# Kernel tuning notes

Hardware: AMD Instinct MI355X
Metric: run time of the kernel (lower is better)

Reference implementation:

```python
import jax, jax.numpy as jnp
import numpy as np

DM = 1024        # model dim
E = 32           # totalexperts = expertsets*nexperts = 8*4
FE = 128         # expertsize
T = 4            # sparsity = nexperts (tokens per group)
EPS_TIEBREAK = 1e-6


def setup_inputs() -> dict:
    key = jax.random.key(0)
    k0, k1, k2, k3 = jax.random.split(key, 4)
    x = jax.random.normal(k0, (4, 4096, DM), dtype=jnp.float32)
    # fan_in-style inits matching misc.get_init_weight / get_init_bias
    controller = jax.random.normal(k1, (DM, E), dtype=jnp.float32) / np.float32(np.sqrt(DM))
    f1 = jax.random.normal(k2, (DM, E, FE), dtype=jnp.float32) / np.float32(np.sqrt(DM))
    bias = jnp.zeros((E, FE), dtype=jnp.float32)
    f2 = jax.random.normal(k3, (E, FE, DM), dtype=jnp.float32) / np.float32(np.sqrt(E * FE / T))
    return {"x": x, "controller": controller, "f1": f1, "bias": bias, "f2": f2}


def reference(x, controller, f1, bias, f2):
    B, S, d = x.shape
    t = T
    g = S // t
    # '... (b t) d -> ... b t d'
    grouped = x.reshape(B, g, t, d)
    # controller logits: '... t d, d e -> ... t e'
    logits = jnp.einsum('bgtd,de->bgte', grouped, controller)
    # deterministic tie-break offset over the t (slot) axis
    logits = logits + jnp.linspace(0.0, EPS_TIEBREAK, t, dtype=logits.dtype)[:, None]
    # softmax over dim=1 (group axis) as in original
    probs = jax.nn.softmax(logits, axis=1)
    # hard argmax mask over dim=-3 (group axis), scaled by soft probs
    perm = (logits == jnp.max(logits, axis=1, keepdims=True)).astype(x.dtype) * probs
    # expert up-projection with soft permutation: '... t d, d e f, ... t e -> ... e f'
    inner = jnp.einsum('bgtd,def,bgte->bgef', grouped, f1, perm)
    inner = jax.nn.relu(inner + bias)
    # expert down-projection: '... e f, e f d -> ... e d'
    inter = jnp.einsum('bgef,efd->bged', inner, f2)
    # unpermute: '... e d, ... t e -> ... t d'
    res = jnp.einsum('bged,bgte->bgtd', inter, perm)
    return res.reshape(B, S, d)
```

## Files before the change

kernel.cpp:

```cpp
#include <hip/hip_runtime.h>
#include <math.h>


#define DM   1024
#define NE   32
#define FE   128
#define T4   4
#define SS   4096
#define NGRP 1024
#define NROW 512
#define LP_STRIDE (NROW * NGRP)
#define VP_OFF   524288
#define HH_OFF   1572864

__global__ __launch_bounds__(256, 4)
void k_logits(const float* __restrict__ x, const float* __restrict__ ctrl,
              float* __restrict__ Lp, float* __restrict__ out)
{
    const int m      = blockIdx.x;
    const int ks     = blockIdx.y;
    const int tid    = threadIdx.x;
    const int base_s = m * 64;
    const int b      = base_s >> 12;
    const int g0     = (base_s & 4095) >> 2;

    __shared__ float xT[64 * 68];
    __shared__ float cs[64 * 32];

    const int tq = tid & 15;
    const int eg = tid >> 4;

    float acc[4][2];
#pragma unroll
    for (int i = 0; i < 4; ++i) { acc[i][0] = 0.f; acc[i][1] = 0.f; }

    const int row0 = tid >> 2;
    const int f4i  = tid & 3;

    for (int kit = 0; kit < 4; ++kit) {
        const int k0 = ks * 256 + kit * 64;
        __syncthreads();
        {
            const float* xp = x + (size_t)(base_s + row0) * DM + k0;
#pragma unroll
            for (int cr = 0; cr < 4; ++cr) {
                const int col = f4i + cr * 4;
                const float4 v = *(const float4*)(xp + col * 4);
                const int d = col * 4;
                xT[(d + 0) * 68 + row0] = v.x;
                xT[(d + 1) * 68 + row0] = v.y;
                xT[(d + 2) * 68 + row0] = v.z;
                xT[(d + 3) * 68 + row0] = v.w;
            }
        }
        {
            const float4* cg = (const float4*)(ctrl + (size_t)k0 * NE);
            float4* cl = (float4*)cs;
            cl[tid]       = cg[tid];
            cl[tid + 256] = cg[tid + 256];
        }
        __syncthreads();
#pragma unroll 8
        for (int d = 0; d < 64; ++d) {
            const float4 xv = *(const float4*)(xT + d * 68 + tq * 4);
            const float2 cv = *(const float2*)(cs + d * 32 + eg * 2);
            const float xa[4] = { xv.x, xv.y, xv.z, xv.w };
#pragma unroll
            for (int i = 0; i < 4; ++i) {
                acc[i][0] += xa[i] * cv.x;
                acc[i][1] += xa[i] * cv.y;
            }
        }
    }

    {
        float* Lb = Lp + (size_t)ks * LP_STRIDE;
        const int g = g0 + tq;
#pragma unroll
        for (int i = 0; i < 4; ++i)
#pragma unroll
            for (int j = 0; j < 2; ++j) {
                const int row = (b * T4 + i) * NE + eg * 2 + j;
                Lb[(size_t)row * NGRP + g] = acc[i][j];
            }
    }

    {
        const float4 z = make_float4(0.f, 0.f, 0.f, 0.f);
        float4* o4 = (float4*)(out + (size_t)(base_s + ks * 16) * DM);
#pragma unroll 4
        for (int i = tid; i < 16 * DM / 4; i += 256) o4[i] = z;
    }
}

__global__ __launch_bounds__(128)
void k_route(float* __restrict__ Lp)
{
    const int r    = blockIdx.x * 2 + (threadIdx.x >> 6);
    const int lane = threadIdx.x & 63;
    const float* L0 = Lp + (size_t)r * NGRP;

    float mx = -INFINITY, s = 0.f;
    int gm = 0;
#pragma unroll
    for (int c = 0; c < 4; ++c) {
        const int g0c = c * 256 + lane * 4;
        const float4 v0 = *(const float4*)(L0 + g0c);
        const float4 v1 = *(const float4*)(L0 + 1 * LP_STRIDE + g0c);
        const float4 v2 = *(const float4*)(L0 + 2 * LP_STRIDE + g0c);
        const float4 v3 = *(const float4*)(L0 + 3 * LP_STRIDE + g0c);
        const float l[4] = { v0.x + v1.x + v2.x + v3.x,
                             v0.y + v1.y + v2.y + v3.y,
                             v0.z + v1.z + v2.z + v3.z,
                             v0.w + v1.w + v2.w + v3.w };
#pragma unroll
        for (int j = 0; j < 4; ++j) {
            const float lv = l[j];
            if (lv > mx) { s = s * __expf(mx - lv) + 1.f; mx = lv; gm = g0c + j; }
            else         { s += __expf(lv - mx); }
        }
    }
#pragma unroll
    for (int off = 1; off < 64; off <<= 1) {
        const float m2 = __shfl_xor(mx, off);
        const float s2 = __shfl_xor(s, off);
        const int   g2 = __shfl_xor(gm, off);
        const float mn = fmaxf(mx, m2);
        s  = s * __expf(mx - mn) + s2 * __expf(m2 - mn);
        gm = (m2 > mx) ? g2 : ((m2 == mx && g2 < gm) ? g2 : gm);
        mx = mn;
    }
    if (lane == 0) {
        ((int*)Lp)[(size_t)r * NGRP] = gm;
        Lp[(size_t)r * NGRP + 1] = 1.f / s;
    }
}

__global__ __launch_bounds__(256, 4)
void k_up(const float* __restrict__ x, const float* __restrict__ f1,
          float* __restrict__ ws)
{
    const int e   = blockIdx.x & 31;
    const int dc  = (blockIdx.x >> 5) & 15;
    const int rh  = blockIdx.x >> 9;
    const int tid = threadIdx.x;

    __shared__ float xs[8 * 68];
    __shared__ int   gS[8];

    if (tid < 8) {
        const int r = (rh * 8 + tid) * NE + e;
        gS[tid] = ((const int*)ws)[(size_t)r * NGRP];
    }
    __syncthreads();

    if (tid < 128) {
        const int row = tid >> 4;
        const int f4c = tid & 15;
        const int grow = rh * 8 + row;
        const int bq = grow >> 2, t = grow & 3;
        const int s = bq * SS + gS[row] * 4 + t;
        const float4 v = *(const float4*)(x + (size_t)s * DM + dc * 64 + f4c * 4);
        xs[row * 68 + f4c * 4 + 0] = v.x;
        xs[row * 68 + f4c * 4 + 1] = v.y;
        xs[row * 68 + f4c * 4 + 2] = v.z;
        xs[row * 68 + f4c * 4 + 3] = v.w;
    }
    __syncthreads();

    const int f4 = tid & 31;
    const int rw = tid >> 5;
    const float* f1p = f1 + (size_t)(dc * 64) * (NE * FE) + e * FE + f4 * 4;
    const float* xp  = xs + rw * 68;

    float a[4] = {0.f, 0.f, 0.f, 0.f};
#pragma unroll 16
    for (int dl = 0; dl < 64; ++dl) {
        const float4 w4 = *(const float4*)(f1p + (size_t)dl * (NE * FE));
        const float xa = xp[dl];
        a[0] += xa * w4.x; a[1] += xa * w4.y; a[2] += xa * w4.z; a[3] += xa * w4.w;
    }

    float* Vp = ws + VP_OFF + (size_t)(dc * 32 + e) * (16 * FE);
    *(float4*)(Vp + (rh * 8 + rw) * FE + f4 * 4) = make_float4(a[0], a[1], a[2], a[3]);
}

__global__ __launch_bounds__(256, 4)
void k_act(const float* __restrict__ bias, float* __restrict__ ws)
{
    const int e   = blockIdx.x & 31;
    const int b   = blockIdx.x >> 5;
    const int tid = threadIdx.x;

    __shared__ float vv[T4][FE];
    __shared__ int   gS[T4];
    __shared__ float pS[T4];

    if (tid < 4) {
        const int r = (b * T4 + tid) * NE + e;
        gS[tid] = ((const int*)ws)[(size_t)r * NGRP];
        pS[tid] = ws[(size_t)r * NGRP + 1];
    }

    const float* Vp = ws + VP_OFF;
#pragma unroll
    for (int q = 0; q < 2; ++q) {
        const int idx = tid + q * 256;
        const int t = idx >> 7, f = idx & 127;
        float s = 0.f;
#pragma unroll
        for (int dc = 0; dc < 16; ++dc)
            s += Vp[(size_t)(dc * 32 + e) * (16 * FE) + (b * T4 + t) * FE + f];
        vv[t][f] = s;
    }
    __syncthreads();

#pragma unroll
    for (int q = 0; q < 2; ++q) {
        const int idx = tid + q * 256;
        const int t = idx >> 7, f = idx & 127;
        float u = bias[e * FE + f];
#pragma unroll
        for (int t2 = 0; t2 < T4; ++t2)
            if (gS[t2] == gS[t]) u += pS[t2] * vv[t2][f];
        ws[HH_OFF + (size_t)e * (16 * FE) + (b * T4 + t) * FE + f] =
            pS[t] * fmaxf(u, 0.f);
    }
}

__global__ __launch_bounds__(256, 2)
void k_down(const float* __restrict__ f2, const float* __restrict__ ws,
            float* __restrict__ out)
{
    const int e   = blockIdx.x & 31;
    const int dt  = (blockIdx.x >> 5) & 7;
    const int rh  = blockIdx.x >> 8;
    const int tid = threadIdx.x;

    __shared__ float hs[8 * FE];
    __shared__ int   gS[8];

    if (tid < 8) {
        const int r = (rh * 8 + tid) * NE + e;
        gS[tid] = ((const int*)ws)[(size_t)r * NGRP];
    }
    {
        const int row = tid >> 5, f4 = tid & 31;
        const float4 v = *(const float4*)(ws + HH_OFF + (size_t)e * (16 * FE)
                                             + (rh * 8 + row) * FE + f4 * 4);
        *(float4*)(hs + row * FE + f4 * 4) = v;
    }
    __syncthreads();

    const int d4 = tid & 31;
    const int rw = tid >> 5;
    const float* f2p = f2 + (size_t)e * FE * DM + dt * 128 + d4 * 4;
    const float* hp  = hs + rw * FE;

    float a[4] = {0.f, 0.f, 0.f, 0.f};
#pragma unroll 16
    for (int f = 0; f < FE; ++f) {
        const float4 w4 = *(const float4*)(f2p + (size_t)f * DM);
        const float ha = hp[f];
        a[0] += ha * w4.x; a[1] += ha * w4.y; a[2] += ha * w4.z; a[3] += ha * w4.w;
    }

    const int grow = rh * 8 + rw;
    const int bq = grow >> 2, t = grow & 3;
    float* orow = out + ((size_t)(bq * SS + gS[rw] * 4 + t)) * DM + dt * 128 + d4 * 4;
    atomicAdd(orow + 0, a[0]);
    atomicAdd(orow + 1, a[1]);
    atomicAdd(orow + 2, a[2]);
    atomicAdd(orow + 3, a[3]);
}

extern "C" void kernel_launch(void* const* d_in, const int* in_sizes, int n_in,
                              void* d_out, int out_size, void* d_ws, size_t ws_size,
                              hipStream_t stream)
{
    const float* x    = (const float*)d_in[0];
    const float* ctrl = (const float*)d_in[1];
    const float* f1   = (const float*)d_in[2];
    const float* bias = (const float*)d_in[3];
    const float* f2   = (const float*)d_in[4];
    float* out = (float*)d_out;
    float* ws  = (float*)d_ws;

    k_logits<<<dim3(256, 4), 256, 0, stream>>>(x, ctrl, ws, out);
    k_route <<<dim3(256),    128, 0, stream>>>(ws);
    k_up    <<<dim3(1024),   256, 0, stream>>>(x, f1, ws);
    k_act   <<<dim3(128),    256, 0, stream>>>(bias, ws);
    k_down  <<<dim3(512),    256, 0, stream>>>(f2, ws, out);
}
```

Baseline: 193.1 us.

## Fuse activation into down-projection, retile logits with prefetch, split route blocks

Removes the separate k_act kernel by having each k_down block reduce the partial up-projection sums, apply the soft-permutation mix, bias and ReLU into shared memory before the down-projection. k_logits now computes 128 rows by 4 experts per thread group and register-prefetches the next x/controller tile, so global loads overlap the previous tile's compute. k_route runs one row per 64-thread block. The fusion repeats the activation reduction across the 8 dt blocks per expert, and the larger logits tile halves the number of blocks and raises register use.

```diff
diff --git a/kernel.cpp b/kernel.cpp
--- a/kernel.cpp
+++ b/kernel.cpp
@@ -11,65 +11,93 @@
 #define NROW 512
 #define LP_STRIDE (NROW * NGRP)
 #define VP_OFF   524288
-#define HH_OFF   1572864
-
-__global__ __launch_bounds__(256, 4)
+
+__global__ __launch_bounds__(256, 2)
 void k_logits(const float* __restrict__ x, const float* __restrict__ ctrl,
               float* __restrict__ Lp, float* __restrict__ out)
 {
     const int m      = blockIdx.x;
     const int ks     = blockIdx.y;
     const int tid    = threadIdx.x;
-    const int base_s = m * 64;
+    const int base_s = m * 128;
     const int b      = base_s >> 12;
     const int g0     = (base_s & 4095) >> 2;
 
-    __shared__ float xT[64 * 68];
+    __shared__ float xT[64 * 132];
     __shared__ float cs[64 * 32];
 
-    const int tq = tid & 15;
-    const int eg = tid >> 4;
-
-    float acc[4][2];
-#pragma unroll
-    for (int i = 0; i < 4; ++i) { acc[i][0] = 0.f; acc[i][1] = 0.f; }
+    const int tq = tid & 31;
+    const int eg = tid >> 5;
+
+    float acc[4][4];
+#pragma unroll
+    for (int i = 0; i < 4; ++i)
+#pragma unroll
+        for (int j = 0; j < 4; ++j) acc[i][j] = 0.f;
 
     const int row0 = tid >> 2;
     const int f4i  = tid & 3;
 
+    float4 px[2][4];
+    float4 pc[2];
+
+    {
+        const int k0 = ks * 256;
+#pragma unroll
+        for (int rr = 0; rr < 2; ++rr) {
+            const float* xp = x + (size_t)(base_s + row0 + rr * 64) * DM + k0;
+#pragma unroll
+            for (int cr = 0; cr < 4; ++cr)
+                px[rr][cr] = *(const float4*)(xp + (f4i + cr * 4) * 4);
+        }
+        const float4* cg = (const float4*)(ctrl + (size_t)k0 * NE);
+        pc[0] = cg[tid]; pc[1] = cg[tid + 256];
+    }
+
     for (int kit = 0; kit < 4; ++kit) {
-        const int k0 = ks * 256 + kit * 64;
         __syncthreads();
+#pragma unroll
+        for (int rr = 0; rr < 2; ++rr) {
+            const int row = row0 + rr * 64;
+#pragma unroll
+            for (int cr = 0; cr < 4; ++cr) {
+                const int d = (f4i + cr * 4) * 4;
+                const float4 v = px[rr][cr];
+                xT[(d + 0) * 132 + row] = v.x;
+                xT[(d + 1) * 132 + row] = v.y;
+                xT[(d + 2) * 132 + row] = v.z;
+                xT[(d + 3) * 132 + row] = v.w;
+            }
+        }
         {
-            const float* xp = x + (size_t)(base_s + row0) * DM + k0;
-#pragma unroll
-            for (int cr = 0; cr < 4; ++cr) {
-                const int col = f4i + cr * 4;
-                const float4 v = *(const float4*)(xp + col * 4);
-                const int d = col * 4;
-                xT[(d + 0) * 68 + row0] = v.x;
-                xT[(d + 1) * 68 + row0] = v.y;
-                xT[(d + 2) * 68 + row0] = v.z;
-                xT[(d + 3) * 68 + row0] = v.w;
+            float4* cl = (float4*)cs;
+            cl[tid] = pc[0]; cl[tid + 256] = pc[1];
+        }
+        __syncthreads();
+
+        if (kit < 3) {
+            const int k0 = ks * 256 + (kit + 1) * 64;
+#pragma unroll
+            for (int rr = 0; rr < 2; ++rr) {
+                const float* xp = x + (size_t)(base_s + row0 + rr * 64) * DM + k0;
+#pragma unroll
+                for (int cr = 0; cr < 4; ++cr)
+                    px[rr][cr] = *(const float4*)(xp + (f4i + cr * 4) * 4);
             }
-        }
-        {
             const float4* cg = (const float4*)(ctrl + (size_t)k0 * NE);
-            float4* cl = (float4*)cs;
-            cl[tid]       = cg[tid];
-            cl[tid + 256] = cg[tid + 256];
-        }
-        __syncthreads();
-#pragma unroll 8
+            pc[0] = cg[tid]; pc[1] = cg[tid + 256];
+        }
+
+#pragma unroll 4
         for (int d = 0; d < 64; ++d) {
-            const float4 xv = *(const float4*)(xT + d * 68 + tq * 4);
-            const float2 cv = *(const float2*)(cs + d * 32 + eg * 2);
+            const float4 xv = *(const float4*)(xT + d * 132 + tq * 4);
+            const float4 cv = *(const float4*)(cs + d * 32 + eg * 4);
             const float xa[4] = { xv.x, xv.y, xv.z, xv.w };
-#pragma unroll
-            for (int i = 0; i < 4; ++i) {
-                acc[i][0] += xa[i] * cv.x;
-                acc[i][1] += xa[i] * cv.y;
-            }
+            const float ca[4] = { cv.x, cv.y, cv.z, cv.w };
+#pragma unroll
+            for (int i = 0; i < 4; ++i)
+#pragma unroll
+                for (int j = 0; j < 4; ++j) acc[i][j] += xa[i] * ca[j];
         }
     }
 
@@ -79,25 +107,25 @@
 #pragma unroll
         for (int i = 0; i < 4; ++i)
 #pragma unroll
-            for (int j = 0; j < 2; ++j) {
-                const int row = (b * T4 + i) * NE + eg * 2 + j;
+            for (int j = 0; j < 4; ++j) {
+                const int row = (b * T4 + i) * NE + eg * 4 + j;
                 Lb[(size_t)row * NGRP + g] = acc[i][j];
             }
     }
 
     {
         const float4 z = make_float4(0.f, 0.f, 0.f, 0.f);
-        float4* o4 = (float4*)(out + (size_t)(base_s + ks * 16) * DM);
+        float4* o4 = (float4*)(out + (size_t)(base_s + ks * 32) * DM);
 #pragma unroll 4
-        for (int i = tid; i < 16 * DM / 4; i += 256) o4[i] = z;
-    }
-}
-
-__global__ __launch_bounds__(128)
+        for (int i = tid; i < 32 * DM / 4; i += 256) o4[i] = z;
+    }
+}
+
+__global__ __launch_bounds__(64)
 void k_route(float* __restrict__ Lp)
 {
-    const int r    = blockIdx.x * 2 + (threadIdx.x >> 6);
-    const int lane = threadIdx.x & 63;
+    const int r    = blockIdx.x;
+    const int lane = threadIdx.x;
     const float* L0 = Lp + (size_t)r * NGRP;
 
     float mx = -INFINITY, s = 0.f;
@@ -185,77 +213,59 @@
     *(float4*)(Vp + (rh * 8 + rw) * FE + f4 * 4) = make_float4(a[0], a[1], a[2], a[3]);
 }
 
-__global__ __launch_bounds__(256, 4)
-void k_act(const float* __restrict__ bias, float* __restrict__ ws)
-{
-    const int e   = blockIdx.x & 31;
-    const int b   = blockIdx.x >> 5;
-    const int tid = threadIdx.x;
-
-    __shared__ float vv[T4][FE];
-    __shared__ int   gS[T4];
-    __shared__ float pS[T4];
-
-    if (tid < 4) {
-        const int r = (b * T4 + tid) * NE + e;
-        gS[tid] = ((const int*)ws)[(size_t)r * NGRP];
-        pS[tid] = ws[(size_t)r * NGRP + 1];
-    }
-
-    const float* Vp = ws + VP_OFF;
-#pragma unroll
-    for (int q = 0; q < 2; ++q) {
-        const int idx = tid + q * 256;
-        const int t = idx >> 7, f = idx & 127;
-        float s = 0.f;
-#pragma unroll
-        for (int dc = 0; dc < 16; ++dc)
-            s += Vp[(size_t)(dc * 32 + e) * (16 * FE) + (b * T4 + t) * FE + f];
-        vv[t][f] = s;
-    }
-    __syncthreads();
-
-#pragma unroll
-    for (int q = 0; q < 2; ++q) {
-        const int idx = tid + q * 256;
-        const int t = idx >> 7, f = idx & 127;
-        float u = bias[e * FE + f];
-#pragma unroll
-        for (int t2 = 0; t2 < T4; ++t2)
-            if (gS[t2] == gS[t]) u += pS[t2] * vv[t2][f];
-        ws[HH_OFF + (size_t)e * (16 * FE) + (b * T4 + t) * FE + f] =
-            pS[t] * fmaxf(u, 0.f);
-    }
-}
-
 __global__ __launch_bounds__(256, 2)
-void k_down(const float* __restrict__ f2, const float* __restrict__ ws,
-            float* __restrict__ out)
+void k_down(const float* __restrict__ f2, const float* __restrict__ bias,
+            const float* __restrict__ ws, float* __restrict__ out)
 {
     const int e   = blockIdx.x & 31;
     const int dt  = (blockIdx.x >> 5) & 7;
     const int rh  = blockIdx.x >> 8;
     const int tid = threadIdx.x;
 
-    __shared__ float hs[8 * FE];
+    __shared__ float vv[8 * 132];
+    __shared__ float hs[8 * 132];
     __shared__ int   gS[8];
+    __shared__ float pS[8];
 
     if (tid < 8) {
         const int r = (rh * 8 + tid) * NE + e;
         gS[tid] = ((const int*)ws)[(size_t)r * NGRP];
-    }
-    {
+        pS[tid] = ws[(size_t)r * NGRP + 1];
+    }
+
+    {
+        const float* Vp = ws + VP_OFF;
         const int row = tid >> 5, f4 = tid & 31;
-        const float4 v = *(const float4*)(ws + HH_OFF + (size_t)e * (16 * FE)
-                                             + (rh * 8 + row) * FE + f4 * 4);
-        *(float4*)(hs + row * FE + f4 * 4) = v;
+        float4 s = make_float4(0.f, 0.f, 0.f, 0.f);
+#pragma unroll
+        for (int dc = 0; dc < 16; ++dc) {
+            const float4 v = *(const float4*)(Vp + (size_t)(dc * 32 + e) * (16 * FE)
+                                                 + (rh * 8 + row) * FE + f4 * 4);
+            s.x += v.x; s.y += v.y; s.z += v.z; s.w += v.w;
+        }
+        *(float4*)(vv + row * 132 + f4 * 4) = s;
+    }
+    __syncthreads();
+
+    {
+#pragma unroll
+        for (int q = 0; q < 4; ++q) {
+            const int idx = tid + q * 256;
+            const int row = idx >> 7, f = idx & 127;
+            const int qb = row & ~3;
+            float u = bias[e * FE + f];
+#pragma unroll
+            for (int t2 = 0; t2 < T4; ++t2)
+                if (gS[qb + t2] == gS[row]) u += pS[qb + t2] * vv[(qb + t2) * 132 + f];
+            hs[row * 132 + f] = pS[row] * fmaxf(u, 0.f);
+        }
     }
     __syncthreads();
 
     const int d4 = tid & 31;
     const int rw = tid >> 5;
     const float* f2p = f2 + (size_t)e * FE * DM + dt * 128 + d4 * 4;
-    const float* hp  = hs + rw * FE;
+    const float* hp  = hs + rw * 132;
 
     float a[4] = {0.f, 0.f, 0.f, 0.f};
 #pragma unroll 16
@@ -286,9 +296,8 @@
     float* out = (float*)d_out;
     float* ws  = (float*)d_ws;
 
-    k_logits<<<dim3(256, 4), 256, 0, stream>>>(x, ctrl, ws, out);
-    k_route <<<dim3(256),    128, 0, stream>>>(ws);
+    k_logits<<<dim3(128, 4), 256, 0, stream>>>(x, ctrl, ws, out);
+    k_route <<<dim3(512),     64, 0, stream>>>(ws);
     k_up    <<<dim3(1024),   256, 0, stream>>>(x, f1, ws);
-    k_act   <<<dim3(128),    256, 0, stream>>>(bias, ws);
-    k_down  <<<dim3(512),    256, 0, stream>>>(f2, ws, out);
-}
+    k_down  <<<dim3(512),    256, 0, stream>>>(f2, bias, ws, out);
+}
```

After: 199.7 us. 1.03x slower.
